# Kernel tuning notes

Hardware: AMD Instinct MI355X
Metric: run time of the kernel (lower is better)

## Reference

```python
import jax, jax.numpy as jnp
import numpy as np

B, MAX_NODE, MEM_LEN, DIM, HEADS, LAYERS, DEG = 32, 1024, 256, 128, 4, 4, 16
CH = DIM // HEADS


def setup_inputs() -> dict:
    key = jax.random.key(0)
    ks = jax.random.split(key, 16)
    counts = np.array([512 + 16 * i for i in range(B)])  # ragged graph sizes, sum = 24320
    N = int(counts.sum())
    node2batch = np.repeat(np.arange(B), counts)
    node2pos = np.concatenate([np.arange(c) for c in counts])
    bmask = np.arange(MAX_NODE)[None, :] < counts[:, None]
    rng = np.random.default_rng(0)
    srcs, dsts, off = [], [], 0
    for c in counts:  # edges stay within each graph
        srcs.append(off + rng.integers(0, c, size=DEG * c))
        dsts.append(off + rng.integers(0, c, size=DEG * c))
        off += c
    edge_index = np.stack([np.concatenate(srcs), np.concatenate(dsts)])

    def rn(k, shape, scale=0.05):
        return jax.random.normal(k, shape, jnp.float32) * scale

    return dict(
        node_feats=rn(ks[0], (N, DIM), 1.0),
        edge_feats=rn(ks[1], (edge_index.shape[1], DIM), 1.0),
        memory=rn(ks[2], (B, MEM_LEN, DIM), 1.0),
        Wn=rn(ks[3], (LAYERS, DIM, DIM)), bn=jnp.zeros((LAYERS, DIM)),
        We=rn(ks[4], (LAYERS, DIM, DIM)),
        att_src=rn(ks[5], (LAYERS, HEADS, CH)),
        att_dst=rn(ks[6], (LAYERS, HEADS, CH)),
        att_edge=rn(ks[7], (LAYERS, HEADS, CH)),
        ln1_g=jnp.ones((LAYERS, DIM)), ln1_b=jnp.zeros((LAYERS, DIM)),
        ln2_g=jnp.ones((LAYERS, DIM)), ln2_b=jnp.zeros((LAYERS, DIM)),
        Wq=rn(ks[8], (LAYERS, DIM, DIM)), Wk=rn(ks[9], (LAYERS, DIM, DIM)),
        Wv=rn(ks[10], (LAYERS, DIM, DIM)), Wo=rn(ks[11], (LAYERS, DIM, DIM)),
        Ew1=rn(ks[12], (LAYERS, 3 * DIM, DIM)), Eb1=jnp.zeros((LAYERS, DIM)),
        Ew2=rn(ks[13], (LAYERS, DIM, DIM)), Eb2=jnp.zeros((LAYERS, DIM)),
        edge_index=jnp.asarray(edge_index, jnp.int32),
        node2batch=jnp.asarray(node2batch, jnp.int32),
        node2pos=jnp.asarray(node2pos, jnp.int32),
        batch_mask=jnp.asarray(bmask),
        mem_pad_mask=jnp.ones((B, MEM_LEN), bool),
    )


def _ln(x, g, b):
    mu = x.mean(-1, keepdims=True)
    v = ((x - mu) ** 2).mean(-1, keepdims=True)
    return (x - mu) * jax.lax.rsqrt(v + 1e-5) * g + b


def reference(node_feats, edge_feats, memory, Wn, bn, We, att_src, att_dst, att_edge,
              ln1_g, ln1_b, ln2_g, ln2_b, Wq, Wk, Wv, Wo, Ew1, Eb1, Ew2, Eb2,
              edge_index, node2batch, node2pos, batch_mask, mem_pad_mask):
    N = node_feats.shape[0]
    src, dst = edge_index[0], edge_index[1]
    # [B, max_node, mem_len]: attend only valid memory slots from valid nodes
    cross_mask = mem_pad_mask[:, None, :] & batch_mask[:, :, None]
    x, e = node_feats, edge_feats
    for l in range(LAYERS):
        # --- edge-conditioned GAT conv (segment softmax over dst) ---
        h = (x @ Wn[l]).reshape(N, HEADS, CH)
        eh = (e @ We[l]).reshape(-1, HEADS, CH)
        logits = (h[src] * att_src[l]).sum(-1) + (h[dst] * att_dst[l]).sum(-1) + (eh * att_edge[l]).sum(-1)
        logits = jax.nn.leaky_relu(logits, 0.2)  # [E, H]
        m = jax.ops.segment_max(logits, dst, num_segments=N)
        ew = jnp.exp(logits - m[dst])
        den = jax.ops.segment_sum(ew, dst, num_segments=N)
        alpha = ew / (den[dst] + 1e-16)
        conv = jax.ops.segment_sum(alpha[..., None] * (h[src] + eh), dst, num_segments=N)
        conv = conv.reshape(N, DIM) + bn[l]
        x = jax.nn.relu(_ln(conv, ln1_g[l], ln1_b[l])) + x
        # --- graph2batch scatter into dense padded tensor ---
        dense = jnp.zeros((B, MAX_NODE, DIM), x.dtype).at[node2batch, node2pos].set(x)
        # --- cross attention against memory ---
        q = (dense @ Wq[l]).reshape(B, MAX_NODE, HEADS, CH)
        k = (memory @ Wk[l]).reshape(B, MEM_LEN, HEADS, CH)
        v = (memory @ Wv[l]).reshape(B, MEM_LEN, HEADS, CH)
        scores = jnp.einsum('bqhc,bkhc->bhqk', q, k) / np.float32(np.sqrt(CH))
        scores = jnp.where(cross_mask[:, None], scores, jnp.float32(-1e9))
        ao = jnp.einsum('bhqk,bkhc->bqhc', jax.nn.softmax(scores, axis=-1), v)
        ao = ao.reshape(B, MAX_NODE, DIM) @ Wo[l]
        dense = jax.nn.relu(_ln(ao + dense, ln2_g[l], ln2_b[l]))
        x = dense[node2batch, node2pos]  # batch2graph gather
        # --- residual sparse edge update ---
        ecat = jnp.concatenate([e, x[src], x[dst]], axis=-1)
        e = e + jax.nn.relu(ecat @ Ew1[l] + Eb1[l]) @ Ew2[l] + Eb2[l]
    return x, e
```

## Files before the change

kernel.cpp:

```cpp
#include <hip/hip_runtime.h>

#define DIM    128
#define HEADS  4
#define CH     32
#define MEMLEN 256
#define LAYERS 4


__global__ void copy_f4(const float4* __restrict__ in, float4* __restrict__ out, long n) {
    long i = (long)blockIdx.x * blockDim.x + threadIdx.x;
    long stride = (long)gridDim.x * blockDim.x;
    for (; i < n; i += stride) out[i] = in[i];
}

__global__ void hist_k(const int* __restrict__ dst, int E, int* __restrict__ deg) {
    int e = blockIdx.x * blockDim.x + threadIdx.x;
    if (e < E) atomicAdd(&deg[dst[e]], 1);
}

__global__ void csr_offsets(const int* __restrict__ deg, int n, int* __restrict__ off) {
    __shared__ int part[1024];
    int t = threadIdx.x;
    int chunk = (n + 1023) >> 10;
    int lo = t * chunk, hi = min(lo + chunk, n);
    int s = 0;
    for (int i = lo; i < hi; i++) s += deg[i];
    part[t] = s; __syncthreads();
    for (int d = 1; d < 1024; d <<= 1) {
        int v = part[t];
        int add = (t >= d) ? part[t - d] : 0;
        __syncthreads();
        part[t] = v + add;
        __syncthreads();
    }
    int run = (t == 0) ? 0 : part[t - 1];
    for (int i = lo; i < hi; i++) { off[i] = run; run += deg[i]; }
    if (t == 1023) off[n] = part[1023];
}

__global__ void csr_fill(const int* __restrict__ dst, int E, const int* __restrict__ off,
                         int* __restrict__ cur, int* __restrict__ csr) {
    int e = blockIdx.x * blockDim.x + threadIdx.x;
    if (e < E) {
        int d = dst[e];
        int p = atomicAdd(&cur[d], 1);
        csr[off[d] + p] = e;
    }
}

__global__ __launch_bounds__(256) void gemm128(const float* __restrict__ A,
                                               const float* __restrict__ W,
                                               const float* __restrict__ bias,
                                               float* __restrict__ out, int R) {
    int r0 = blockIdx.x * 64, t = threadIdx.x;
    __shared__ float at[64][DIM];
    for (int i = t; i < 64 * 32; i += 256) {
        int rr = i >> 5, cc = i & 31;
        if (r0 + rr < R)
            ((float4*)at[rr])[cc] = ((const float4*)(A + (size_t)(r0 + rr) * DIM))[cc];
    }
    __syncthreads();
    int c0 = (t & 31) * 4;
    int rb = (t >> 5) * 8;
    float acc[8][4];
#pragma unroll
    for (int ee = 0; ee < 8; ee++)
        acc[ee][0] = acc[ee][1] = acc[ee][2] = acc[ee][3] = 0.f;
    for (int k = 0; k < DIM; k += 4) {
        float4 w0 = *(const float4*)&W[(k + 0) * DIM + c0];
        float4 w1 = *(const float4*)&W[(k + 1) * DIM + c0];
        float4 w2 = *(const float4*)&W[(k + 2) * DIM + c0];
        float4 w3 = *(const float4*)&W[(k + 3) * DIM + c0];
#pragma unroll
        for (int ee = 0; ee < 8; ee++) {
            float4 a = *(float4*)&at[rb + ee][k];
            acc[ee][0] += a.x * w0.x + a.y * w1.x + a.z * w2.x + a.w * w3.x;
            acc[ee][1] += a.x * w0.y + a.y * w1.y + a.z * w2.y + a.w * w3.y;
            acc[ee][2] += a.x * w0.z + a.y * w1.z + a.z * w2.z + a.w * w3.z;
            acc[ee][3] += a.x * w0.w + a.y * w1.w + a.z * w2.w + a.w * w3.w;
        }
    }
    float4 bb = make_float4(0.f, 0.f, 0.f, 0.f);
    if (bias) bb = *(const float4*)&bias[c0];
#pragma unroll
    for (int ee = 0; ee < 8; ee++) {
        int r = r0 + rb + ee;
        if (r < R) {
            float4 o = make_float4(acc[ee][0] + bb.x, acc[ee][1] + bb.y,
                                   acc[ee][2] + bb.z, acc[ee][3] + bb.w);
            *(float4*)&out[(size_t)r * DIM + c0] = o;
        }
    }
}

__global__ __launch_bounds__(256) void node_proj_tile(
    const float* __restrict__ x, const float* __restrict__ W,
    const float* __restrict__ att_s, const float* __restrict__ att_d,
    float* __restrict__ h, float* __restrict__ ssrc, float* __restrict__ sdst, int N) {
    int r0 = blockIdx.x * 64, t = threadIdx.x;
    __shared__ float at[64][DIM];
    for (int i = t; i < 64 * 32; i += 256) {
        int rr = i >> 5, cc = i & 31;
        if (r0 + rr < N)
            ((float4*)at[rr])[cc] = ((const float4*)(x + (size_t)(r0 + rr) * DIM))[cc];
    }
    __syncthreads();
    int c0 = (t & 31) * 4;
    int rb = (t >> 5) * 8;
    float acc[8][4];
#pragma unroll
    for (int ee = 0; ee < 8; ee++)
        acc[ee][0] = acc[ee][1] = acc[ee][2] = acc[ee][3] = 0.f;
    for (int k = 0; k < DIM; k += 4) {
        float4 w0 = *(const float4*)&W[(k + 0) * DIM + c0];
        float4 w1 = *(const float4*)&W[(k + 1) * DIM + c0];
        float4 w2 = *(const float4*)&W[(k + 2) * DIM + c0];
        float4 w3 = *(const float4*)&W[(k + 3) * DIM + c0];
#pragma unroll
        for (int ee = 0; ee < 8; ee++) {
            float4 a = *(float4*)&at[rb + ee][k];
            acc[ee][0] += a.x * w0.x + a.y * w1.x + a.z * w2.x + a.w * w3.x;
            acc[ee][1] += a.x * w0.y + a.y * w1.y + a.z * w2.y + a.w * w3.y;
            acc[ee][2] += a.x * w0.z + a.y * w1.z + a.z * w2.z + a.w * w3.z;
            acc[ee][3] += a.x * w0.w + a.y * w1.w + a.z * w2.w + a.w * w3.w;
        }
    }
    int hh = (t & 31) >> 3;
    float4 as = *(const float4*)&att_s[c0];
    float4 ad = *(const float4*)&att_d[c0];
#pragma unroll
    for (int ee = 0; ee < 8; ee++) {
        int r = r0 + rb + ee;
        if (r < N) {
            *(float4*)&h[(size_t)r * DIM + c0] =
                make_float4(acc[ee][0], acc[ee][1], acc[ee][2], acc[ee][3]);
            float ps = acc[ee][0]*as.x + acc[ee][1]*as.y + acc[ee][2]*as.z + acc[ee][3]*as.w;
            float pd = acc[ee][0]*ad.x + acc[ee][1]*ad.y + acc[ee][2]*ad.z + acc[ee][3]*ad.w;
#pragma unroll
            for (int mk = 1; mk < 8; mk <<= 1) {
                ps += __shfl_xor(ps, mk, 32);
                pd += __shfl_xor(pd, mk, 32);
            }
            if (((t & 31) & 7) == 0) {
                ssrc[r * HEADS + hh] = ps;
                sdst[r * HEADS + hh] = pd;
            }
        }
    }
}


__global__ void make_waE(const float* __restrict__ We, const float* __restrict__ att_e,
                         float* __restrict__ waE) {
    int k = threadIdx.x;
#pragma unroll
    for (int h = 0; h < HEADS; h++) {
        float s = 0.f;
#pragma unroll
        for (int c = 0; c < CH; c++) s += We[k * DIM + h * CH + c] * att_e[h * CH + c];
        waE[k * HEADS + h] = s;
    }
}

__global__ void sedge_logits(const float* __restrict__ e, const float* __restrict__ waE,
                             const float* __restrict__ ssrc, const float* __restrict__ sdst,
                             const int* __restrict__ src, const int* __restrict__ dst,
                             float* __restrict__ lw, int E) {
    __shared__ float w[DIM * HEADS];
    int t = threadIdx.x;
    w[t] = waE[t]; w[t + 256] = waE[t + 256];
    __syncthreads();
    int g = t >> 5, lane = t & 31;
    int eid = blockIdx.x * 8 + g;
    if (eid >= E) return;
    const float* er = e + (size_t)eid * DIM;
    float s0 = 0.f, s1 = 0.f, s2 = 0.f, s3 = 0.f;
#pragma unroll
    for (int j = 0; j < 4; j++) {
        int k = lane + 32 * j;
        float v = er[k];
        s0 += v * w[k * 4 + 0]; s1 += v * w[k * 4 + 1];
        s2 += v * w[k * 4 + 2]; s3 += v * w[k * 4 + 3];
    }
#pragma unroll
    for (int m = 16; m; m >>= 1) {
        s0 += __shfl_xor(s0, m, 32); s1 += __shfl_xor(s1, m, 32);
        s2 += __shfl_xor(s2, m, 32); s3 += __shfl_xor(s3, m, 32);
    }
    if (lane == 0) {
        int sn = src[eid] * HEADS, dn = dst[eid] * HEADS;
        float l0 = ssrc[sn + 0] + sdst[dn + 0] + s0;
        float l1 = ssrc[sn + 1] + sdst[dn + 1] + s1;
        float l2 = ssrc[sn + 2] + sdst[dn + 2] + s2;
        float l3 = ssrc[sn + 3] + sdst[dn + 3] + s3;
        lw[eid * 4 + 0] = (l0 >= 0.f) ? l0 : 0.2f * l0;
        lw[eid * 4 + 1] = (l1 >= 0.f) ? l1 : 0.2f * l1;
        lw[eid * 4 + 2] = (l2 >= 0.f) ? l2 : 0.2f * l2;
        lw[eid * 4 + 3] = (l3 >= 0.f) ? l3 : 0.2f * l3;
    }
}

__global__ void seg_softmax(const int* __restrict__ off, const int* __restrict__ csr,
                            float* __restrict__ lw, float* __restrict__ den, int NH) {
    int i = blockIdx.x * blockDim.x + threadIdx.x;
    if (i >= NH) return;
    int n = i >> 2, hh = i & 3;
    int o0 = off[n], o1 = off[n + 1];
    float m = -1e30f;
    for (int o = o0; o < o1; o++) m = fmaxf(m, lw[csr[o] * HEADS + hh]);
    float s = 0.f;
    for (int o = o0; o < o1; o++) {
        int idx = csr[o] * HEADS + hh;
        float w = __expf(lw[idx] - m);
        lw[idx] = w;
        s += w;
    }
    den[i] = s;
}

__global__ __launch_bounds__(512) void conv_ln4(
    const int* __restrict__ off, const int* __restrict__ csr, const int* __restrict__ src,
    const float* __restrict__ lw, const float* __restrict__ den,
    const float* __restrict__ hbuf, const float* __restrict__ e, const float* __restrict__ We,
    const float* __restrict__ bn, const float* __restrict__ g, const float* __restrict__ b,
    float* __restrict__ x, int N) {
    int t = threadIdx.x;
    int tt = t & 127, part = t >> 7;
    int n = blockIdx.x;
    int hh = tt >> 5;
    __shared__ float aggeP[4][HEADS][DIM];
    __shared__ float acchP[4][DIM];
    __shared__ float ehcP[4][DIM];
    __shared__ float wred[16];
    int o0 = off[n], o1 = off[n + 1];
    float acch = 0.f, a0 = 0.f, a1 = 0.f, a2 = 0.f, a3 = 0.f;
    for (int o = o0 + part; o < o1; o += 4) {
        int eid = csr[o];
        int s = src[eid];
        float4 al = *(const float4*)&lw[eid * 4];
        acch += ((&al.x)[hh]) * hbuf[(size_t)s * DIM + tt];
        float ev = e[(size_t)eid * DIM + tt];
        a0 += al.x * ev; a1 += al.y * ev; a2 += al.z * ev; a3 += al.w * ev;
    }
    aggeP[part][0][tt] = a0; aggeP[part][1][tt] = a1;
    aggeP[part][2][tt] = a2; aggeP[part][3][tt] = a3;
    acchP[part][tt] = acch;
    __syncthreads();
    float ehc = 0.f;
    int k0 = part * 32;
    for (int k = k0; k < k0 + 32; k++) {
        float ag = aggeP[0][hh][k] + aggeP[1][hh][k] + aggeP[2][hh][k] + aggeP[3][hh][k];
        ehc += ag * We[k * DIM + tt];
    }
    ehcP[part][tt] = ehc;
    __syncthreads();
    float conv = (acchP[0][tt] + acchP[1][tt] + acchP[2][tt] + acchP[3][tt]
                + ehcP[0][tt] + ehcP[1][tt] + ehcP[2][tt] + ehcP[3][tt])
                 / (den[n * HEADS + hh] + 1e-16f) + bn[tt];
    int w = t >> 6;
    float s1 = conv;
#pragma unroll
    for (int mk = 32; mk; mk >>= 1) s1 += __shfl_xor(s1, mk, 64);
    if ((t & 63) == 0) wred[w] = s1;
    __syncthreads();
    float mu = (wred[w] + wred[w ^ 1]) * (1.f / DIM);
    float diff = conv - mu;
    float s2 = diff * diff;
#pragma unroll
    for (int mk = 32; mk; mk >>= 1) s2 += __shfl_xor(s2, mk, 64);
    if ((t & 63) == 0) wred[8 + w] = s2;
    __syncthreads();
    float var = (wred[8 + w] + wred[8 + (w ^ 1)]) * (1.f / DIM);
    if (part == 0) {
        float y = diff * rsqrtf(var + 1e-5f) * g[tt] + b[tt];
        x[(size_t)n * DIM + tt] = fmaxf(y, 0.f) + x[(size_t)n * DIM + tt];
    }
}

__global__ __launch_bounds__(256) void cross_attn_tile(
    float* __restrict__ x, const float* __restrict__ qg,
    const float* __restrict__ kb, const float* __restrict__ vb,
    const float* __restrict__ Wo, const float* __restrict__ g,
    const float* __restrict__ b, const int* __restrict__ boff) {
    int bb = blockIdx.y;
    int n0 = boff[bb] + blockIdx.x * 64;
    int cnt = boff[bb + 1] - n0;
    if (cnt <= 0) return;
    int nq = min(64, cnt);
    int t = threadIdx.x;
    int q = t & 63, h = t >> 6;

    __shared__ float smem[64 * 132];

    float qv[32];
    if (q < nq) {
        const float4* qp = (const float4*)(qg + (size_t)(n0 + q) * DIM + h * CH);
#pragma unroll
        for (int j = 0; j < 8; j++) {
            float4 v = qp[j];
            qv[4*j+0] = v.x; qv[4*j+1] = v.y; qv[4*j+2] = v.z; qv[4*j+3] = v.w;
        }
    } else {
#pragma unroll
        for (int c = 0; c < 32; c++) qv[c] = 0.f;
    }

    float oacc[32];
#pragma unroll
    for (int c = 0; c < 32; c++) oacc[c] = 0.f;
    float m = -1e30f, l = 0.f;

    const float4* Ksrc = (const float4*)(kb + (size_t)bb * MEMLEN * DIM);
    const float4* Vsrc = (const float4*)(vb + (size_t)bb * MEMLEN * DIM);
    float4* Kl = (float4*)smem;
    float4* Vl = (float4*)(smem + 32 * DIM);

    for (int ch = 0; ch < MEMLEN / 32; ch++) {
        __syncthreads();
#pragma unroll
        for (int r = 0; r < 4; r++) {
            int idx = t + r * 256;
            Kl[idx] = Ksrc[ch * 1024 + idx];
            Vl[idx] = Vsrc[ch * 1024 + idx];
        }
        __syncthreads();
        float sc[32];
#pragma unroll
        for (int kk = 0; kk < 32; kk++) {
            const float* kp = smem + kk * DIM + h * CH;
            float s = 0.f;
#pragma unroll
            for (int c = 0; c < 32; c++) s += qv[c] * kp[c];
            sc[kk] = s * 0.17677669529663689f;
        }
        float mc = sc[0];
#pragma unroll
        for (int kk = 1; kk < 32; kk++) mc = fmaxf(mc, sc[kk]);
        float mn = fmaxf(m, mc);
        float scale = __expf(m - mn);
        m = mn;
        float ls = 0.f;
#pragma unroll
        for (int kk = 0; kk < 32; kk++) {
            float w = __expf(sc[kk] - mn);
            sc[kk] = w;
            ls += w;
        }
        l = l * scale + ls;
#pragma unroll
        for (int c = 0; c < 32; c++) oacc[c] *= scale;
#pragma unroll
        for (int kk = 0; kk < 32; kk++) {
            const float* vp = smem + 32 * DIM + kk * DIM + h * CH;
            float w = sc[kk];
#pragma unroll
            for (int c = 0; c < 32; c++) oacc[c] += w * vp[c];
        }
    }
    __syncthreads();
    {
        float inv = 1.f / l;
        float* ap = smem + q * 132 + h * CH;
#pragma unroll
        for (int c = 0; c < 32; c++) ap[c] = oacc[c] * inv;
    }
    __syncthreads();
    int c0 = (t & 31) * 4;
    int rb = (t >> 5) * 8;
    float acc2[8][4];
#pragma unroll
    for (int ee = 0; ee < 8; ee++)
        acc2[ee][0] = acc2[ee][1] = acc2[ee][2] = acc2[ee][3] = 0.f;
    for (int k = 0; k < DIM; k += 4) {
        float4 w0 = *(const float4*)&Wo[(k + 0) * DIM + c0];
        float4 w1 = *(const float4*)&Wo[(k + 1) * DIM + c0];
        float4 w2 = *(const float4*)&Wo[(k + 2) * DIM + c0];
        float4 w3 = *(const float4*)&Wo[(k + 3) * DIM + c0];
#pragma unroll
        for (int ee = 0; ee < 8; ee++) {
            float4 a = *(const float4*)(smem + (rb + ee) * 132 + k);
            acc2[ee][0] += a.x * w0.x + a.y * w1.x + a.z * w2.x + a.w * w3.x;
            acc2[ee][1] += a.x * w0.y + a.y * w1.y + a.z * w2.y + a.w * w3.y;
            acc2[ee][2] += a.x * w0.z + a.y * w1.z + a.z * w2.z + a.w * w3.z;
            acc2[ee][3] += a.x * w0.w + a.y * w1.w + a.z * w2.w + a.w * w3.w;
        }
    }
    float4 gg = *(const float4*)&g[c0];
    float4 bb4 = *(const float4*)&b[c0];
#pragma unroll
    for (int ee = 0; ee < 8; ee++) {
        int r = rb + ee;
        if (r < nq) {
            float4 xr = *(const float4*)&x[(size_t)(n0 + r) * DIM + c0];
            float o0 = acc2[ee][0] + xr.x, o1 = acc2[ee][1] + xr.y;
            float o2 = acc2[ee][2] + xr.z, o3 = acc2[ee][3] + xr.w;
            float s1 = o0 + o1 + o2 + o3;
#pragma unroll
            for (int mk = 16; mk; mk >>= 1) s1 += __shfl_xor(s1, mk, 32);
            float mu = s1 * (1.f / DIM);
            float d0 = o0 - mu, d1 = o1 - mu, d2 = o2 - mu, d3 = o3 - mu;
            float s2 = d0*d0 + d1*d1 + d2*d2 + d3*d3;
#pragma unroll
            for (int mk = 16; mk; mk >>= 1) s2 += __shfl_xor(s2, mk, 32);
            float rs = rsqrtf(s2 * (1.f / DIM) + 1e-5f);
            float4 o = make_float4(fmaxf(d0 * rs * gg.x + bb4.x, 0.f),
                                   fmaxf(d1 * rs * gg.y + bb4.y, 0.f),
                                   fmaxf(d2 * rs * gg.z + bb4.z, 0.f),
                                   fmaxf(d3 * rs * gg.w + bb4.w, 0.f));
            *(float4*)&x[(size_t)(n0 + r) * DIM + c0] = o;
        }
    }
}

__global__ __launch_bounds__(256, 4) void edge_mlp(float* __restrict__ e,
                                                   const float* __restrict__ xs,
                                                   const float* __restrict__ xd,
                                                   const int* __restrict__ src,
                                                   const int* __restrict__ dst,
                                                   const float* __restrict__ W1,
                                                   const float* __restrict__ W2,
                                                   const float* __restrict__ Eb2, int E) {
    int e0 = blockIdx.x * 64, t = threadIdx.x;
    int tx = t & 15, ty = t >> 4;
    int c0 = tx * 8;
    __shared__ float at[64][130];
    for (int i = t; i < 64 * 32; i += 256) {
        int rr = i >> 5, cc = i & 31;
        if (e0 + rr < E)
            *(float4*)&at[rr][cc * 4] = *(const float4*)&e[(size_t)(e0 + rr) * DIM + cc * 4];
    }
    __syncthreads();
    float acc[4][8];
#pragma unroll
    for (int r = 0; r < 4; r++)
#pragma unroll
        for (int c = 0; c < 8; c++) acc[r][c] = 0.f;
    for (int k = 0; k < DIM; k += 4) {
        float4 a4[4];
#pragma unroll
        for (int r = 0; r < 4; r++) a4[r] = *(const float4*)&at[ty * 4 + r][k];
        float4 wv[8];
#pragma unroll
        for (int kk = 0; kk < 4; kk++) {
            wv[2*kk]   = *(const float4*)&W1[(size_t)(k + kk) * DIM + c0];
            wv[2*kk+1] = *(const float4*)&W1[(size_t)(k + kk) * DIM + c0 + 4];
        }
#pragma unroll
        for (int kk = 0; kk < 4; kk++) {
#pragma unroll
            for (int r = 0; r < 4; r++) {
                float av = (&a4[r].x)[kk];
                float4 w0 = wv[2*kk], w1 = wv[2*kk+1];
                acc[r][0] += av * w0.x; acc[r][1] += av * w0.y;
                acc[r][2] += av * w0.z; acc[r][3] += av * w0.w;
                acc[r][4] += av * w1.x; acc[r][5] += av * w1.y;
                acc[r][6] += av * w1.z; acc[r][7] += av * w1.w;
            }
        }
    }
#pragma unroll
    for (int r = 0; r < 4; r++) {
        int row = e0 + ty * 4 + r;
        if (row < E) {
            int sr = src[row], dr = dst[row];
            float4 s0 = *(const float4*)&xs[(size_t)sr * DIM + c0];
            float4 s1 = *(const float4*)&xs[(size_t)sr * DIM + c0 + 4];
            float4 d0 = *(const float4*)&xd[(size_t)dr * DIM + c0];
            float4 d1 = *(const float4*)&xd[(size_t)dr * DIM + c0 + 4];
            acc[r][0] = fmaxf(acc[r][0] + s0.x + d0.x, 0.f);
            acc[r][1] = fmaxf(acc[r][1] + s0.y + d0.y, 0.f);
            acc[r][2] = fmaxf(acc[r][2] + s0.z + d0.z, 0.f);
            acc[r][3] = fmaxf(acc[r][3] + s0.w + d0.w, 0.f);
            acc[r][4] = fmaxf(acc[r][4] + s1.x + d1.x, 0.f);
            acc[r][5] = fmaxf(acc[r][5] + s1.y + d1.y, 0.f);
            acc[r][6] = fmaxf(acc[r][6] + s1.z + d1.z, 0.f);
            acc[r][7] = fmaxf(acc[r][7] + s1.w + d1.w, 0.f);
        }
    }
    __syncthreads();
#pragma unroll
    for (int r = 0; r < 4; r++) {
        *(float4*)&at[ty * 4 + r][c0]     = make_float4(acc[r][0], acc[r][1], acc[r][2], acc[r][3]);
        *(float4*)&at[ty * 4 + r][c0 + 4] = make_float4(acc[r][4], acc[r][5], acc[r][6], acc[r][7]);
    }
    __syncthreads();
#pragma unroll
    for (int r = 0; r < 4; r++)
#pragma unroll
        for (int c = 0; c < 8; c++) acc[r][c] = 0.f;
    for (int k = 0; k < DIM; k += 4) {
        float4 a4[4];
#pragma unroll
        for (int r = 0; r < 4; r++) a4[r] = *(const float4*)&at[ty * 4 + r][k];
        float4 wv[8];
#pragma unroll
        for (int kk = 0; kk < 4; kk++) {
            wv[2*kk]   = *(const float4*)&W2[(size_t)(k + kk) * DIM + c0];
            wv[2*kk+1] = *(const float4*)&W2[(size_t)(k + kk) * DIM + c0 + 4];
        }
#pragma unroll
        for (int kk = 0; kk < 4; kk++) {
#pragma unroll
            for (int r = 0; r < 4; r++) {
                float av = (&a4[r].x)[kk];
                float4 w0 = wv[2*kk], w1 = wv[2*kk+1];
                acc[r][0] += av * w0.x; acc[r][1] += av * w0.y;
                acc[r][2] += av * w0.z; acc[r][3] += av * w0.w;
                acc[r][4] += av * w1.x; acc[r][5] += av * w1.y;
                acc[r][6] += av * w1.z; acc[r][7] += av * w1.w;
            }
        }
    }
    float4 b20 = *(const float4*)&Eb2[c0];
    float4 b21 = *(const float4*)&Eb2[c0 + 4];
#pragma unroll
    for (int r = 0; r < 4; r++) {
        int row = e0 + ty * 4 + r;
        if (row < E) {
            float4 o0 = *(const float4*)&e[(size_t)row * DIM + c0];
            float4 o1 = *(const float4*)&e[(size_t)row * DIM + c0 + 4];
            o0.x += acc[r][0] + b20.x; o0.y += acc[r][1] + b20.y;
            o0.z += acc[r][2] + b20.z; o0.w += acc[r][3] + b20.w;
            o1.x += acc[r][4] + b21.x; o1.y += acc[r][5] + b21.y;
            o1.z += acc[r][6] + b21.z; o1.w += acc[r][7] + b21.w;
            *(float4*)&e[(size_t)row * DIM + c0]     = o0;
            *(float4*)&e[(size_t)row * DIM + c0 + 4] = o1;
        }
    }
}


extern "C" void kernel_launch(void* const* d_in, const int* in_sizes, int n_in,
                              void* d_out, int out_size, void* d_ws, size_t ws_size,
                              hipStream_t stream) {
    const float* node_feats = (const float*)d_in[0];
    const float* edge_feats = (const float*)d_in[1];
    const float* memory     = (const float*)d_in[2];
    const float* Wn   = (const float*)d_in[3];
    const float* bn   = (const float*)d_in[4];
    const float* We   = (const float*)d_in[5];
    const float* att_src  = (const float*)d_in[6];
    const float* att_dst  = (const float*)d_in[7];
    const float* att_edge = (const float*)d_in[8];
    const float* ln1_g = (const float*)d_in[9];
    const float* ln1_b = (const float*)d_in[10];
    const float* ln2_g = (const float*)d_in[11];
    const float* ln2_b = (const float*)d_in[12];
    const float* Wq = (const float*)d_in[13];
    const float* Wk = (const float*)d_in[14];
    const float* Wv = (const float*)d_in[15];
    const float* Wo = (const float*)d_in[16];
    const float* Ew1 = (const float*)d_in[17];
    const float* Eb1 = (const float*)d_in[18];
    const float* Ew2 = (const float*)d_in[19];
    const float* Eb2 = (const float*)d_in[20];
    const int* edge_index = (const int*)d_in[21];
    const int* node2batch = (const int*)d_in[22];

    const int N = in_sizes[0] / DIM;
    const int E = in_sizes[1] / DIM;
    const int Bn = in_sizes[2] / (MEMLEN * DIM);
    const int* srcA = edge_index;
    const int* dstA = edge_index + E;

    float* x = (float*)d_out;
    float* e = x + (size_t)N * DIM;

    char* p = (char*)d_ws;
    auto carve = [&](size_t bytes) {
        void* r = (void*)p;
        p += (bytes + 255) & ~(size_t)255;
        return r;
    };
    float* h     = (float*)carve((size_t)N * DIM * 4);
    float* qg    = (float*)carve((size_t)N * DIM * 4);
    float* xs    = (float*)carve((size_t)N * DIM * 4);
    float* xd    = (float*)carve((size_t)N * DIM * 4);
    float* ssrc  = (float*)carve((size_t)N * HEADS * 4);
    float* sdst  = (float*)carve((size_t)N * HEADS * 4);
    float* lw    = (float*)carve((size_t)E * HEADS * 4);
    float* den   = (float*)carve((size_t)N * HEADS * 4);
    float* waE   = (float*)carve((size_t)DIM * HEADS * 4);
    float* kbuf  = (float*)carve((size_t)Bn * MEMLEN * DIM * 4);
    float* vbuf  = (float*)carve((size_t)Bn * MEMLEN * DIM * 4);
    int* deg     = (int*)carve((size_t)N * 4);
    int* cur     = (int*)carve((size_t)N * 4);
    int* off     = (int*)carve(((size_t)N + 1) * 4);
    int* csr     = (int*)carve((size_t)E * 4);
    int* bcnt    = (int*)carve((size_t)Bn * 4);
    int* boff    = (int*)carve(((size_t)Bn + 1) * 4);

    {
        long nx = (long)N * DIM / 4;
        copy_f4<<<dim3(2048), dim3(256), 0, stream>>>((const float4*)node_feats, (float4*)x, nx);
        long nen = (long)E * DIM / 4;
        copy_f4<<<dim3(4096), dim3(256), 0, stream>>>((const float4*)edge_feats, (float4*)e, nen);
    }

    hipMemsetAsync(deg, 0, (size_t)N * 4, stream);
    hipMemsetAsync(cur, 0, (size_t)N * 4, stream);
    hipMemsetAsync(bcnt, 0, (size_t)Bn * 4, stream);
    hist_k<<<dim3((E + 255) / 256), dim3(256), 0, stream>>>(dstA, E, deg);
    csr_offsets<<<dim3(1), dim3(1024), 0, stream>>>(deg, N, off);
    csr_fill<<<dim3((E + 255) / 256), dim3(256), 0, stream>>>(dstA, E, off, cur, csr);
    hist_k<<<dim3((N + 255) / 256), dim3(256), 0, stream>>>(node2batch, N, bcnt);
    csr_offsets<<<dim3(1), dim3(1024), 0, stream>>>(bcnt, Bn, boff);

    const int mrows = Bn * MEMLEN;
    const int maxTiles = 1024 / 64;
    for (int l = 0; l < LAYERS; l++) {
        const float* Wn_l  = Wn  + (size_t)l * DIM * DIM;
        const float* We_l  = We  + (size_t)l * DIM * DIM;
        const float* Wq_l  = Wq  + (size_t)l * DIM * DIM;
        const float* Wk_l  = Wk  + (size_t)l * DIM * DIM;
        const float* Wv_l  = Wv  + (size_t)l * DIM * DIM;
        const float* Wo_l  = Wo  + (size_t)l * DIM * DIM;
        const float* Ew1_l = Ew1 + (size_t)l * 3 * DIM * DIM;
        const float* Ew2_l = Ew2 + (size_t)l * DIM * DIM;

        node_proj_tile<<<dim3((N + 63) / 64), dim3(256), 0, stream>>>(
            x, Wn_l, att_src + l * DIM, att_dst + l * DIM, h, ssrc, sdst, N);
        make_waE<<<dim3(1), dim3(DIM), 0, stream>>>(We_l, att_edge + l * DIM, waE);
        sedge_logits<<<dim3((E + 7) / 8), dim3(256), 0, stream>>>(
            e, waE, ssrc, sdst, srcA, dstA, lw, E);
        seg_softmax<<<dim3((N * HEADS + 255) / 256), dim3(256), 0, stream>>>(
            off, csr, lw, den, N * HEADS);
        conv_ln4<<<dim3(N), dim3(512), 0, stream>>>(
            off, csr, srcA, lw, den, h, e, We_l,
            bn + l * DIM, ln1_g + l * DIM, ln1_b + l * DIM, x, N);
        gemm128<<<dim3((mrows + 63) / 64), dim3(256), 0, stream>>>(
            memory, Wk_l, nullptr, kbuf, mrows);
        gemm128<<<dim3((mrows + 63) / 64), dim3(256), 0, stream>>>(
            memory, Wv_l, nullptr, vbuf, mrows);
        gemm128<<<dim3((N + 63) / 64), dim3(256), 0, stream>>>(
            x, Wq_l, nullptr, qg, N);
        cross_attn_tile<<<dim3(maxTiles, Bn), dim3(256), 0, stream>>>(
            x, qg, kbuf, vbuf, Wo_l, ln2_g + l * DIM, ln2_b + l * DIM, boff);
        gemm128<<<dim3((N + 63) / 64), dim3(256), 0, stream>>>(
            x, Ew1_l + (size_t)DIM * DIM, Eb1 + l * DIM, xs, N);
        gemm128<<<dim3((N + 63) / 64), dim3(256), 0, stream>>>(
            x, Ew1_l + (size_t)2 * DIM * DIM, nullptr, xd, N);
        edge_mlp<<<dim3((E + 63) / 64), dim3(256), 0, stream>>>(
            e, xs, xd, srcA, dstA, Ew1_l, Ew2_l, Eb2 + l * DIM, E);
    }
}
```

Measured before the change: 4.336 ms.

## Enlarge edge MLP tile to 128 rows and fuse paired projection GEMMs

```diff
diff --git a/kernel.cpp b/kernel.cpp
--- a/kernel.cpp
+++ b/kernel.cpp
@@ -89,6 +89,64 @@
             float4 o = make_float4(acc[ee][0] + bb.x, acc[ee][1] + bb.y,
                                    acc[ee][2] + bb.z, acc[ee][3] + bb.w);
             *(float4*)&out[(size_t)r * DIM + c0] = o;
+        }
+    }
+}
+
+__global__ __launch_bounds__(256, 2) void gemm128_dual(const float* __restrict__ A,
+                                                       const float* __restrict__ Wa,
+                                                       const float* __restrict__ Wb,
+                                                       const float* __restrict__ biasA,
+                                                       float* __restrict__ outA,
+                                                       float* __restrict__ outB, int R) {
+    int r0 = blockIdx.x * 64, t = threadIdx.x;
+    __shared__ float at[64][DIM];
+    for (int i = t; i < 64 * 32; i += 256) {
+        int rr = i >> 5, cc = i & 31;
+        if (r0 + rr < R)
+            ((float4*)at[rr])[cc] = ((const float4*)(A + (size_t)(r0 + rr) * DIM))[cc];
+    }
+    __syncthreads();
+    int c0 = (t & 31) * 4;
+    int rb = (t >> 5) * 8;
+    float accA[8][4], accB[8][4];
+#pragma unroll
+    for (int ee = 0; ee < 8; ee++)
+#pragma unroll
+        for (int j = 0; j < 4; j++) { accA[ee][j] = 0.f; accB[ee][j] = 0.f; }
+    for (int k = 0; k < DIM; k += 4) {
+        float4 wa0 = *(const float4*)&Wa[(k + 0) * DIM + c0];
+        float4 wa1 = *(const float4*)&Wa[(k + 1) * DIM + c0];
+        float4 wa2 = *(const float4*)&Wa[(k + 2) * DIM + c0];
+        float4 wa3 = *(const float4*)&Wa[(k + 3) * DIM + c0];
+        float4 wb0 = *(const float4*)&Wb[(k + 0) * DIM + c0];
+        float4 wb1 = *(const float4*)&Wb[(k + 1) * DIM + c0];
+        float4 wb2 = *(const float4*)&Wb[(k + 2) * DIM + c0];
+        float4 wb3 = *(const float4*)&Wb[(k + 3) * DIM + c0];
+#pragma unroll
+        for (int ee = 0; ee < 8; ee++) {
+            float4 a = *(float4*)&at[rb + ee][k];
+            accA[ee][0] += a.x * wa0.x + a.y * wa1.x + a.z * wa2.x + a.w * wa3.x;
+            accA[ee][1] += a.x * wa0.y + a.y * wa1.y + a.z * wa2.y + a.w * wa3.y;
+            accA[ee][2] += a.x * wa0.z + a.y * wa1.z + a.z * wa2.z + a.w * wa3.z;
+            accA[ee][3] += a.x * wa0.w + a.y * wa1.w + a.z * wa2.w + a.w * wa3.w;
+            accB[ee][0] += a.x * wb0.x + a.y * wb1.x + a.z * wb2.x + a.w * wb3.x;
+            accB[ee][1] += a.x * wb0.y + a.y * wb1.y + a.z * wb2.y + a.w * wb3.y;
+            accB[ee][2] += a.x * wb0.z + a.y * wb1.z + a.z * wb2.z + a.w * wb3.z;
+            accB[ee][3] += a.x * wb0.w + a.y * wb1.w + a.z * wb2.w + a.w * wb3.w;
+        }
+    }
+    float4 bb = make_float4(0.f, 0.f, 0.f, 0.f);
+    if (biasA) bb = *(const float4*)&biasA[c0];
+#pragma unroll
+    for (int ee = 0; ee < 8; ee++) {
+        int r = r0 + rb + ee;
+        if (r < R) {
+            *(float4*)&outA[(size_t)r * DIM + c0] =
+                make_float4(accA[ee][0] + bb.x, accA[ee][1] + bb.y,
+                            accA[ee][2] + bb.z, accA[ee][3] + bb.w);
+            *(float4*)&outB[(size_t)r * DIM + c0] =
+                make_float4(accB[ee][0], accB[ee][1], accB[ee][2], accB[ee][3]);
         }
     }
 }
@@ -412,7 +470,7 @@
     }
 }
 
-__global__ __launch_bounds__(256, 4) void edge_mlp(float* __restrict__ e,
+__global__ __launch_bounds__(256, 2) void edge_mlp(float* __restrict__ e,
                                                    const float* __restrict__ xs,
                                                    const float* __restrict__ xd,
                                                    const int* __restrict__ src,
@@ -420,37 +478,32 @@
                                                    const float* __restrict__ W1,
                                                    const float* __restrict__ W2,
                                                    const float* __restrict__ Eb2, int E) {
-    int e0 = blockIdx.x * 64, t = threadIdx.x;
+    int e0 = blockIdx.x * 128, t = threadIdx.x;
     int tx = t & 15, ty = t >> 4;
     int c0 = tx * 8;
-    __shared__ float at[64][130];
-    for (int i = t; i < 64 * 32; i += 256) {
+    __shared__ float at[128][132];
+    for (int i = t; i < 128 * 32; i += 256) {
         int rr = i >> 5, cc = i & 31;
         if (e0 + rr < E)
             *(float4*)&at[rr][cc * 4] = *(const float4*)&e[(size_t)(e0 + rr) * DIM + cc * 4];
     }
     __syncthreads();
-    float acc[4][8];
-#pragma unroll
-    for (int r = 0; r < 4; r++)
+    float acc[8][8];
+#pragma unroll
+    for (int r = 0; r < 8; r++)
 #pragma unroll
         for (int c = 0; c < 8; c++) acc[r][c] = 0.f;
     for (int k = 0; k < DIM; k += 4) {
-        float4 a4[4];
-#pragma unroll
-        for (int r = 0; r < 4; r++) a4[r] = *(const float4*)&at[ty * 4 + r][k];
-        float4 wv[8];
+        float4 a4[8];
+#pragma unroll
+        for (int r = 0; r < 8; r++) a4[r] = *(const float4*)&at[r * 16 + ty][k];
 #pragma unroll
         for (int kk = 0; kk < 4; kk++) {
-            wv[2*kk]   = *(const float4*)&W1[(size_t)(k + kk) * DIM + c0];
-            wv[2*kk+1] = *(const float4*)&W1[(size_t)(k + kk) * DIM + c0 + 4];
-        }
-#pragma unroll
-        for (int kk = 0; kk < 4; kk++) {
-#pragma unroll
-            for (int r = 0; r < 4; r++) {
+            float4 w0 = *(const float4*)&W1[(size_t)(k + kk) * DIM + c0];
+            float4 w1 = *(const float4*)&W1[(size_t)(k + kk) * DIM + c0 + 4];
+#pragma unroll
+            for (int r = 0; r < 8; r++) {
                 float av = (&a4[r].x)[kk];
-                float4 w0 = wv[2*kk], w1 = wv[2*kk+1];
                 acc[r][0] += av * w0.x; acc[r][1] += av * w0.y;
                 acc[r][2] += av * w0.z; acc[r][3] += av * w0.w;
                 acc[r][4] += av * w1.x; acc[r][5] += av * w1.y;
@@ -459,8 +512,8 @@
         }
     }
 #pragma unroll
-    for (int r = 0; r < 4; r++) {
-        int row = e0 + ty * 4 + r;
+    for (int r = 0; r < 8; r++) {
+        int row = e0 + r * 16 + ty;
         if (row < E) {
             int sr = src[row], dr = dst[row];
             float4 s0 = *(const float4*)&xs[(size_t)sr * DIM + c0];
@@ -479,31 +532,26 @@
     }
     __syncthreads();
 #pragma unroll
-    for (int r = 0; r < 4; r++) {
-        *(float4*)&at[ty * 4 + r][c0]     = make_float4(acc[r][0], acc[r][1], acc[r][2], acc[r][3]);
-        *(float4*)&at[ty * 4 + r][c0 + 4] = make_float4(acc[r][4], acc[r][5], acc[r][6], acc[r][7]);
-    }
-    __syncthreads();
-#pragma unroll
-    for (int r = 0; r < 4; r++)
+    for (int r = 0; r < 8; r++) {
+        *(float4*)&at[r * 16 + ty][c0]     = make_float4(acc[r][0], acc[r][1], acc[r][2], acc[r][3]);
+        *(float4*)&at[r * 16 + ty][c0 + 4] = make_float4(acc[r][4], acc[r][5], acc[r][6], acc[r][7]);
+    }
+    __syncthreads();
+#pragma unroll
+    for (int r = 0; r < 8; r++)
 #pragma unroll
         for (int c = 0; c < 8; c++) acc[r][c] = 0.f;
     for (int k = 0; k < DIM; k += 4) {
-        float4 a4[4];
-#pragma unroll
-        for (int r = 0; r < 4; r++) a4[r] = *(const float4*)&at[ty * 4 + r][k];
-        float4 wv[8];
+        float4 a4[8];
+#pragma unroll
+        for (int r = 0; r < 8; r++) a4[r] = *(const float4*)&at[r * 16 + ty][k];
 #pragma unroll
         for (int kk = 0; kk < 4; kk++) {
-            wv[2*kk]   = *(const float4*)&W2[(size_t)(k + kk) * DIM + c0];
-            wv[2*kk+1] = *(const float4*)&W2[(size_t)(k + kk) * DIM + c0 + 4];
-        }
-#pragma unroll
-        for (int kk = 0; kk < 4; kk++) {
-#pragma unroll
-            for (int r = 0; r < 4; r++) {
+            float4 w0 = *(const float4*)&W2[(size_t)(k + kk) * DIM + c0];
+            float4 w1 = *(const float4*)&W2[(size_t)(k + kk) * DIM + c0 + 4];
+#pragma unroll
+            for (int r = 0; r < 8; r++) {
                 float av = (&a4[r].x)[kk];
-                float4 w0 = wv[2*kk], w1 = wv[2*kk+1];
                 acc[r][0] += av * w0.x; acc[r][1] += av * w0.y;
                 acc[r][2] += av * w0.z; acc[r][3] += av * w0.w;
                 acc[r][4] += av * w1.x; acc[r][5] += av * w1.y;
@@ -514,8 +562,8 @@
     float4 b20 = *(const float4*)&Eb2[c0];
     float4 b21 = *(const float4*)&Eb2[c0 + 4];
 #pragma unroll
-    for (int r = 0; r < 4; r++) {
-        int row = e0 + ty * 4 + r;
+    for (int r = 0; r < 8; r++) {
+        int row = e0 + r * 16 + ty;
         if (row < E) {
             float4 o0 = *(const float4*)&e[(size_t)row * DIM + c0];
             float4 o1 = *(const float4*)&e[(size_t)row * DIM + c0 + 4];
@@ -628,19 +676,16 @@
         conv_ln4<<<dim3(N), dim3(512), 0, stream>>>(
             off, csr, srcA, lw, den, h, e, We_l,
             bn + l * DIM, ln1_g + l * DIM, ln1_b + l * DIM, x, N);
-        gemm128<<<dim3((mrows + 63) / 64), dim3(256), 0, stream>>>(
-            memory, Wk_l, nullptr, kbuf, mrows);
-        gemm128<<<dim3((mrows + 63) / 64), dim3(256), 0, stream>>>(
-            memory, Wv_l, nullptr, vbuf, mrows);
+        gemm128_dual<<<dim3((mrows + 63) / 64), dim3(256), 0, stream>>>(
+            memory, Wk_l, Wv_l, nullptr, kbuf, vbuf, mrows);
         gemm128<<<dim3((N + 63) / 64), dim3(256), 0, stream>>>(
             x, Wq_l, nullptr, qg, N);
         cross_attn_tile<<<dim3(maxTiles, Bn), dim3(256), 0, stream>>>(
             x, qg, kbuf, vbuf, Wo_l, ln2_g + l * DIM, ln2_b + l * DIM, boff);
-        gemm128<<<dim3((N + 63) / 64), dim3(256), 0, stream>>>(
-            x, Ew1_l + (size_t)DIM * DIM, Eb1 + l * DIM, xs, N);
-        gemm128<<<dim3((N + 63) / 64), dim3(256), 0, stream>>>(
-            x, Ew1_l + (size_t)2 * DIM * DIM, nullptr, xd, N);
-        edge_mlp<<<dim3((E + 63) / 64), dim3(256), 0, stream>>>(
+        gemm128_dual<<<dim3((N + 63) / 64), dim3(256), 0, stream>>>(
+            x, Ew1_l + (size_t)DIM * DIM, Ew1_l + (size_t)2 * DIM * DIM,
+            Eb1 + l * DIM, xs, xd, N);
+        edge_mlp<<<dim3((E + 127) / 128), dim3(256), 0, stream>>>(
             e, xs, xd, srcA, dstA, Ew1_l, Ew2_l, Eb2 + l * DIM, E);
     }
 }
```

New measurement: 4.150 ms. 1.04x faster.
